# Performance work log

Measured on AMD Instinct MI355X. Metric: run time of the kernel, lower is better.

Reference implementation:

```python
import jax, jax.numpy as jnp
import numpy as np
import math

N = 50000   # nodes
E = 800000  # edges
D = 64      # in_feat_dim == out_feat_dim
T = 8       # num node types
R = 8       # num relations
SQRT_DK = math.sqrt(D)


def typed_matmul(x, W, types, num_types):
    """Row-wise x[i] @ W[types[i]] without materializing [E, D, D] gathered weights."""
    out = jnp.zeros((x.shape[0], W.shape[-1]), x.dtype)
    for t in range(num_types):
        out = out + jnp.where((types == t)[:, None], x @ W[t], 0.0)
    return out


def segment_softmax(score, index, num_segments):
    smax = jax.ops.segment_max(score, index, num_segments=num_segments)
    ex = jnp.exp(score - smax[index])
    ssum = jax.ops.segment_sum(ex, index, num_segments=num_segments)
    return ex / (ssum[index] + 1e-16)


def setup_inputs() -> dict:
    key = jax.random.key(0)
    ks = jax.random.split(key, 10)
    h = jax.random.normal(ks[0], (N, D), dtype=jnp.float32)
    adj = jax.random.randint(ks[1], (2, E), 0, N, dtype=jnp.int64)
    edge_type = jax.random.randint(ks[2], (E,), 0, R, dtype=jnp.int64)
    node_type = jax.random.randint(ks[3], (N,), 0, T, dtype=jnp.int64)
    k_weights = jax.random.uniform(ks[4], (T, D, D), dtype=jnp.float32)
    q_weights = jax.random.uniform(ks[5], (T, D, D), dtype=jnp.float32)
    v_weights = jax.random.uniform(ks[6], (T, D, D), dtype=jnp.float32)
    a_weights = jax.random.uniform(ks[7], (T, D, D), dtype=jnp.float32)
    relation_att = jax.random.uniform(ks[8], (R, D, D), dtype=jnp.float32)
    relation_msg = jax.random.uniform(ks[9], (R, D, D), dtype=jnp.float32)
    relation_pri = jnp.ones((R, 1), dtype=jnp.float32)
    skip = jnp.ones((T,), dtype=jnp.float32)
    return {
        "h": h, "adj": adj, "edge_type": edge_type, "node_type": node_type,
        "src_type": 0, "dst_type": 0,
        "k_weights": k_weights, "q_weights": q_weights, "v_weights": v_weights,
        "a_weights": a_weights, "relation_pri": relation_pri,
        "relation_att": relation_att, "relation_msg": relation_msg, "skip": skip,
    }


def reference(h, adj, edge_type, node_type, src_type, dst_type,
              k_weights, q_weights, v_weights, a_weights,
              relation_pri, relation_att, relation_msg, skip):
    src = adj[0]  # _j side (messages come from src)
    dst = adj[1]  # _i side (scatter/softmax index)

    # Node-type-indexed projections (done per node, then gathered per edge --
    # identical math to the per-edge bmm in the original).
    k_node = typed_matmul(h, k_weights, node_type, T)  # [N, D]
    q_node = typed_matmul(h, q_weights, node_type, T)
    v_node = typed_matmul(h, v_weights, node_type, T)

    # Relation-indexed per-edge transforms.
    k = typed_matmul(k_node[src], relation_att, edge_type, R)  # [E, D]
    v = typed_matmul(v_node[src], relation_msg, edge_type, R)  # [E, D]
    q = q_node[dst]                                            # [E, D]

    attn_score = jnp.sum(k * q, axis=1, keepdims=True) * relation_pri[edge_type] / SQRT_DK  # [E, 1]
    alpha = segment_softmax(attn_score, dst, N)  # edge softmax over incoming edges
    rst = v * alpha                              # [E, D]

    agg = jax.ops.segment_sum(rst, dst, num_segments=N)  # [N, D]

    # Update: node-type-indexed output transform scaled by sigmoid(skip[type]).
    trans_out = typed_matmul(agg, a_weights, node_type, T)
    alpha_skip = jax.nn.sigmoid(skip[node_type])
    return trans_out * alpha_skip[:, None]
```

## Files before the change

kernel.cpp:

```cpp
#include <hip/hip_runtime.h>
#include <math.h>

typedef float f32x4 __attribute__((ext_vector_type(4)));
typedef short bf16x8 __attribute__((ext_vector_type(8)));
typedef _Float16 f16x8 __attribute__((ext_vector_type(8)));
typedef _Float16 f16x4 __attribute__((ext_vector_type(4)));

#define D 64
#define TT 8
#define RR 8

#define SCAN_TPB 256
#define SCAN_CH 4
#define SCAN_ELEMS (SCAN_TPB * SCAN_CH)

#define HIST_CH 8
#define SCAT_CH 4
#define SCORE_XB 256
#define V2_XB 64
#define AGG_XB 256

__device__ __forceinline__ float bf2f(unsigned short u) {
    union { unsigned int i; float f; } x;
    x.i = ((unsigned int)u) << 16;
    return x.f;
}
__device__ __forceinline__ unsigned short f2bf(float f) {
    union { float f; unsigned int i; } x;
    x.f = f;
    unsigned int i = x.i;
    unsigned int r = (i + 0x7FFFu + ((i >> 16) & 1u)) >> 16;
    return (unsigned short)r;
}
struct BfPair { short hi; short lo; };
__device__ __forceinline__ BfPair split2(float x) {
    BfPair p;
    unsigned short h = f2bf(x);
    p.hi = (short)h;
    p.lo = (short)f2bf(x - bf2f(h));
    return p;
}
__device__ __forceinline__ void load_A_split(const float* __restrict__ p, bf16x8& ah, bf16x8& al) {
#pragma unroll
    for (int i = 0; i < 8; ++i) {
        BfPair s = split2(p[i]);
        ah[i] = s.hi; al[i] = s.lo;
    }
}
__device__ __forceinline__ void load_B_split(const float* __restrict__ W, int ks, int c, int lane,
                                             bf16x8& bh, bf16x8& bl) {
    int n = lane & 15, q = lane >> 4;
#pragma unroll
    for (int i = 0; i < 8; ++i) {
        BfPair s = split2(W[(ks * 32 + q * 8 + i) * 64 + c * 16 + n]);
        bh[i] = s.hi; bl[i] = s.lo;
    }
}
__device__ __forceinline__ void load_B_split_f16(const float* __restrict__ W, int ks, int c, int lane,
                                                 f16x8& bh, f16x8& bl) {
    int n = lane & 15, q = lane >> 4;
#pragma unroll
    for (int i = 0; i < 8; ++i) {
        float w = W[(ks * 32 + q * 8 + i) * 64 + c * 16 + n];
        _Float16 h = (_Float16)w;
        bh[i] = h;
        bl[i] = (_Float16)(w - (float)h);
    }
}
__device__ __forceinline__ f16x8 load_B_frag_f16(const float* __restrict__ W, int ks, int c, int lane) {
    int n = lane & 15, q = lane >> 4;
    f16x8 r;
#pragma unroll
    for (int i = 0; i < 8; ++i)
        r[i] = (_Float16)W[(ks * 32 + q * 8 + i) * 64 + c * 16 + n];
    return r;
}

#define MFMA16(a, b, c) __builtin_amdgcn_mfma_f32_16x16x32_bf16(a, b, c, 0, 0, 0)
#define MFMAH(a, b, c)  __builtin_amdgcn_mfma_f32_16x16x32_f16(a, b, c, 0, 0, 0)

#define SPLIT_MFMA_BODY(acc, A0h, A0l, A1h, A1l, Bh, Bl)          \
    _Pragma("unroll")                                             \
    for (int c = 0; c < 4; ++c) {                                 \
        acc[c] = MFMA16(A0h, Bh[0][c], acc[c]);                   \
        acc[c] = MFMA16(A0l, Bh[0][c], acc[c]);                   \
        acc[c] = MFMA16(A0h, Bl[0][c], acc[c]);                   \
        acc[c] = MFMA16(A1h, Bh[1][c], acc[c]);                   \
        acc[c] = MFMA16(A1l, Bh[1][c], acc[c]);                   \
        acc[c] = MFMA16(A1h, Bl[1][c], acc[c]);                   \
    }

__global__ void hist_kernel(const int* __restrict__ dst, const int* __restrict__ et,
                            const int* __restrict__ nt,
                            int* __restrict__ deg, int* __restrict__ tcnt, int* __restrict__ rcnt,
                            int* __restrict__ erank, int N, int E) {
    __shared__ int l_r[RR], l_t[TT];
    if (threadIdx.x < RR) l_r[threadIdx.x] = 0;
    if (threadIdx.x < TT) l_t[threadIdx.x] = 0;
    __syncthreads();
    const int stride = gridDim.x * blockDim.x;
    const int tid = blockIdx.x * blockDim.x + threadIdx.x;
#pragma unroll
    for (int i = 0; i < HIST_CH; ++i) {
        int e = tid + i * stride;
        if (e < E) {
            erank[e] = atomicAdd(&deg[dst[e]], 1);
            atomicAdd(&l_r[et[e]], 1);
        }
    }
#pragma unroll
    for (int i = 0; i < HIST_CH; ++i) {
        int n = tid + i * stride;
        if (n < N) atomicAdd(&l_t[nt[n]], 1);
    }
    __syncthreads();
    if (threadIdx.x < RR && l_r[threadIdx.x]) atomicAdd(&rcnt[threadIdx.x], l_r[threadIdx.x]);
    if (threadIdx.x < TT && l_t[threadIdx.x]) atomicAdd(&tcnt[threadIdx.x], l_t[threadIdx.x]);
}

__global__ void scan_sum_kernel(const int* __restrict__ deg, int* __restrict__ bsum, int N) {
    __shared__ int ws[SCAN_TPB / 64];
    int tid = threadIdx.x;
    int base = blockIdx.x * SCAN_ELEMS + tid * SCAN_CH;
    int s = 0;
#pragma unroll
    for (int i = 0; i < SCAN_CH; ++i) {
        int idx = base + i;
        if (idx < N) s += deg[idx];
    }
#pragma unroll
    for (int d = 32; d; d >>= 1) s += __shfl_xor(s, d, 64);
    if ((tid & 63) == 0) ws[tid >> 6] = s;
    __syncthreads();
    if (tid == 0) {
        int t = 0;
#pragma unroll
        for (int i = 0; i < SCAN_TPB / 64; ++i) t += ws[i];
        bsum[blockIdx.x] = t;
    }
}
__global__ void scan_out_kernel(const int* __restrict__ deg, const int* __restrict__ bsum, int nsb,
                                int* __restrict__ off, int N, int Etot,
                                const int* __restrict__ tcnt, int* __restrict__ toff, int* __restrict__ tcur,
                                const int* __restrict__ rcnt, int* __restrict__ roff, int* __restrict__ rcur) {
    __shared__ int ts[SCAN_TPB];
    __shared__ int bb;
    int tid = threadIdx.x;
    if (tid < 64) {
        int v = 0;
        if (nsb <= 64) {
            v = (tid < nsb && tid < blockIdx.x) ? bsum[tid] : 0;
#pragma unroll
            for (int d = 32; d; d >>= 1) v += __shfl_xor(v, d, 64);
        } else if (tid == 0) {
            for (int b = 0; b < blockIdx.x; ++b) v += bsum[b];
        }
        if (tid == 0) bb = v;
    }
    if (blockIdx.x == 0 && tid == 1) {
        int a = 0;
        for (int t = 0; t < TT; ++t) { toff[t] = a; tcur[t] = a; a += tcnt[t]; }
        toff[TT] = a;
        int b2 = 0;
        for (int r = 0; r < RR; ++r) { roff[r] = b2; rcur[r] = b2; b2 += rcnt[r]; }
        roff[RR] = b2;
        off[N] = Etot;
    }
    int base = blockIdx.x * SCAN_ELEMS + tid * SCAN_CH;
    int loc[SCAN_CH];
    int s = 0;
#pragma unroll
    for (int i = 0; i < SCAN_CH; ++i) {
        int idx = base + i;
        int v = (idx < N) ? deg[idx] : 0;
        loc[i] = v; s += v;
    }
    ts[tid] = s;
    __syncthreads();
    for (int sh = 1; sh < SCAN_TPB; sh <<= 1) {
        int v = (tid >= sh) ? ts[tid - sh] : 0;
        __syncthreads();
        ts[tid] += v;
        __syncthreads();
    }
    int run = bb + ((tid > 0) ? ts[tid - 1] : 0);
#pragma unroll
    for (int i = 0; i < SCAN_CH; ++i) {
        int idx = base + i;
        if (idx < N) { off[idx] = run; run += loc[i]; }
    }
}

__global__ void scatter_kernel(const int* __restrict__ src, const int* __restrict__ dst,
                               const int* __restrict__ et, const int* __restrict__ nt,
                               const int* __restrict__ offs, const int* __restrict__ erank,
                               int* __restrict__ tcur, int* __restrict__ rcur,
                               int* __restrict__ rsrc, int* __restrict__ rdst,
                               int* __restrict__ rdpos, int* __restrict__ nidx, int N, int E) {
    __shared__ int l_r[RR], l_t[TT], base_r[RR], base_t[TT];
    if (threadIdx.x < RR) l_r[threadIdx.x] = 0;
    if (threadIdx.x < TT) l_t[threadIdx.x] = 0;
    __syncthreads();
    const int stride = gridDim.x * blockDim.x;
    const int tid = blockIdx.x * blockDim.x + threadIdx.x;
    int s[SCAT_CH], d[SCAT_CH], r[SCAT_CH], rrank[SCAT_CH];
    int t[SCAT_CH], trank[SCAT_CH];
#pragma unroll
    for (int i = 0; i < SCAT_CH; ++i) {
        int e = tid + i * stride;
        if (e < E) {
            s[i] = src[e]; d[i] = dst[e]; r[i] = et[e];
            rrank[i] = atomicAdd(&l_r[r[i]], 1);
        }
        int n = tid + i * stride;
        if (n < N) {
            t[i] = nt[n];
            trank[i] = atomicAdd(&l_t[t[i]], 1);
        }
    }
    __syncthreads();
    if (threadIdx.x < RR)
        base_r[threadIdx.x] = l_r[threadIdx.x] ? atomicAdd(&rcur[threadIdx.x], l_r[threadIdx.x]) : 0;
    if (threadIdx.x < TT)
        base_t[threadIdx.x] = l_t[threadIdx.x] ? atomicAdd(&tcur[threadIdx.x], l_t[threadIdx.x]) : 0;
    __syncthreads();
#pragma unroll
    for (int i = 0; i < SCAT_CH; ++i) {
        int e = tid + i * stride;
        if (e < E) {
            int pos = offs[d[i]] + erank[e];
            int rp = base_r[r[i]] + rrank[i];
            rsrc[rp] = s[i]; rdst[rp] = d[i]; rdpos[rp] = pos;
        }
        int n = tid + i * stride;
        if (n < N) nidx[base_t[t[i]] + trank[i]] = n;
    }
}

__global__ void proj_kernel(const float* __restrict__ h,
                            const float* __restrict__ Wk, const float* __restrict__ Wq,
                            const float* __restrict__ Wv,
                            const int* __restrict__ toff, const int* __restrict__ nidx,
                            _Float16* __restrict__ kh16,
                            _Float16* __restrict__ qout, _Float16* __restrict__ vout) {
    const int t = blockIdx.z, a = blockIdx.y, lane = threadIdx.x;
    const int beg = toff[t], end = toff[t + 1], cnt = end - beg;
    if (cnt <= 0) return;
    const int nstrips = (cnt + 15) >> 4;
    const float* W = (a == 0 ? Wk : (a == 1 ? Wq : Wv)) + (size_t)t * 4096;
    const int m = lane & 15, quad = lane >> 4;

    bf16x8 Bh[2][4], Bl[2][4];
#pragma unroll
    for (int ks = 0; ks < 2; ++ks)
#pragma unroll
        for (int c = 0; c < 4; ++c) load_B_split(W, ks, c, lane, Bh[ks][c], Bl[ks][c]);

    _Float16* out = (a == 0) ? kh16 : (a == 1 ? qout : vout);

    for (int s = blockIdx.x; s < nstrips; s += gridDim.x) {
        int base = beg + s * 16;
        int rA = base + m; if (rA > end - 1) rA = end - 1;
        const float* hp = h + (size_t)nidx[rA] * D;
        bf16x8 A0h, A0l, A1h, A1l;
        load_A_split(hp + quad * 8, A0h, A0l);
        load_A_split(hp + 32 + quad * 8, A1h, A1l);
        f32x4 acc[4];
#pragma unroll
        for (int c = 0; c < 4; ++c) acc[c] = (f32x4){0.f, 0.f, 0.f, 0.f};
        SPLIT_MFMA_BODY(acc, A0h, A0l, A1h, A1l, Bh, Bl)
#pragma unroll
        for (int reg = 0; reg < 4; ++reg) {
            int rr = base + quad * 4 + reg;
            if (rr < end) {
                int nid = nidx[rr];
#pragma unroll
                for (int c = 0; c < 4; ++c)
                    out[(size_t)nid * D + c * 16 + m] = (_Float16)acc[c][reg];
            }
        }
    }
}

__global__ void score_v2_kernel(const int* __restrict__ rsrc, const int* __restrict__ rdst,
                                const int* __restrict__ rdpos, const int* __restrict__ roff,
                                const _Float16* __restrict__ kh16,
                                const _Float16* __restrict__ qn, const float* __restrict__ Aatt,
                                const float* __restrict__ pri, int2* __restrict__ rec,
                                const _Float16* __restrict__ vn, const float* __restrict__ Amsg,
                                _Float16* __restrict__ V2, int N) {
    const int r = blockIdx.y;
    const int lane = threadIdx.x & 63;
    const int wv = threadIdx.x >> 6;
    const int m = lane & 15, quad = lane >> 4;

    if (blockIdx.x >= SCORE_XB) {
        const int g = (blockIdx.x - SCORE_XB) * 4 + wv;
        const int nstrips = (N + 15) >> 4;
        const float* W = Amsg + (size_t)r * 4096;
        f16x8 B[2][4];
#pragma unroll
        for (int ks = 0; ks < 2; ++ks)
#pragma unroll
            for (int c = 0; c < 4; ++c) B[ks][c] = load_B_frag_f16(W, ks, c, lane);

        for (int s = g; s < nstrips; s += V2_XB * 4) {
            int base = s * 16;
            int rA = base + m; if (rA > N - 1) rA = N - 1;
            f16x8 A0 = *(const f16x8*)(vn + (size_t)rA * D + quad * 8);
            f16x8 A1 = *(const f16x8*)(vn + (size_t)rA * D + 32 + quad * 8);
            f32x4 acc[4];
#pragma unroll
            for (int c = 0; c < 4; ++c) acc[c] = (f32x4){0.f, 0.f, 0.f, 0.f};
#pragma unroll
            for (int c = 0; c < 4; ++c) {
                acc[c] = MFMAH(A0, B[0][c], acc[c]);
                acc[c] = MFMAH(A1, B[1][c], acc[c]);
            }
#pragma unroll
            for (int reg = 0; reg < 4; ++reg) {
                int rr = base + quad * 4 + reg;
                if (rr < N) {
#pragma unroll
                    for (int c = 0; c < 4; ++c)
                        V2[((size_t)rr * RR + r) * D + c * 16 + m] = (_Float16)acc[c][reg];
                }
            }
        }
        return;
    }

    const int beg = roff[r], end = roff[r + 1], cnt = end - beg;
    if (cnt <= 0) return;
    const int nstrips = (cnt + 15) >> 4;
    const float scale = pri[r] * 0.125f;
    const float* W = Aatt + (size_t)r * 4096;

    f16x8 Bh[2][4], Bl[2][4];
#pragma unroll
    for (int ks = 0; ks < 2; ++ks)
#pragma unroll
        for (int c = 0; c < 4; ++c) load_B_split_f16(W, ks, c, lane, Bh[ks][c], Bl[ks][c]);

    const int g = blockIdx.x * 4 + wv;
    for (int st = g; st < nstrips; st += SCORE_XB * 4) {
        int base = st * 16;
        int ia = base + m; if (ia > cnt - 1) ia = cnt - 1;
        int s = rsrc[beg + ia];
        const _Float16* kr = kh16 + (size_t)s * D;
        f16x8 A0 = *(const f16x8*)(kr + quad * 8);
        f16x8 A1 = *(const f16x8*)(kr + 32 + quad * 8);
        f32x4 acc[4];
#pragma unroll
        for (int c = 0; c < 4; ++c) acc[c] = (f32x4){0.f, 0.f, 0.f, 0.f};
#pragma unroll
        for (int c = 0; c < 4; ++c) {
            acc[c] = MFMAH(A0, Bh[0][c], acc[c]);
            acc[c] = MFMAH(A0, Bl[0][c], acc[c]);
            acc[c] = MFMAH(A1, Bh[1][c], acc[c]);
            acc[c] = MFMAH(A1, Bl[1][c], acc[c]);
        }

        float p4[4];
#pragma unroll
        for (int reg = 0; reg < 4; ++reg) {
            int ie = base + quad * 4 + reg; if (ie > cnt - 1) ie = cnt - 1;
            const _Float16* qp = qn + (size_t)rdst[beg + ie] * D + m;
            float pr = acc[0][reg] * (float)qp[0] + acc[1][reg] * (float)qp[16]
                     + acc[2][reg] * (float)qp[32] + acc[3][reg] * (float)qp[48];
#pragma unroll
            for (int d = 8; d; d >>= 1) pr += __shfl_xor(pr, d, 64);
            p4[reg] = pr;
        }
        if (m < 4) {
            int idx = base + quad * 4 + m;
            if (idx < cnt) {
                float v = (m == 0) ? p4[0] : (m == 1) ? p4[1] : (m == 2) ? p4[2] : p4[3];
                int sagain = rsrc[beg + idx];
                int2 rc;
                rc.x = __float_as_int(v * scale);
                rc.y = (sagain << 3) | r;
                rec[rdpos[beg + idx]] = rc;
            }
        }
    }
}

__global__ void agg_out_kernel(const int* __restrict__ offs, const int2* __restrict__ rec,
                               const _Float16* __restrict__ V2,
                               const float* __restrict__ Wa, const float* __restrict__ skp,
                               const int* __restrict__ toff, const int* __restrict__ nidx,
                               float* __restrict__ out) {
    const int t = blockIdx.y;
    const int beg = toff[t], end = toff[t + 1], cnt = end - beg;
    if (cnt <= 0) return;
    const int nstrips = (cnt + 15) >> 4;
    const int lane = threadIdx.x & 63;
    const int wv = threadIdx.x >> 6;
    const int quad = lane >> 4, ql = lane & 15;
    const int q16 = wv * 4 + quad;
    const int qb = quad << 4;
    const int m = lane & 15, qd = lane >> 4;
    const float sg = 1.f / (1.f + __expf(-skp[t]));

    __shared__ float As[16][68];

    bf16x8 Bh2[2], Bl2[2];
    const float* W = Wa + (size_t)t * 4096;
#pragma unroll
    for (int ks = 0; ks < 2; ++ks) load_B_split(W, ks, wv, lane, Bh2[ks], Bl2[ks]);

    for (int s = blockIdx.x; s < nstrips; s += gridDim.x) {
        int base = beg + s * 16;
        int rr = base + q16; if (rr > end - 1) rr = end - 1;
        int i = nidx[rr];
        const int ebeg = offs[i], eend = offs[i + 1];
        float mmax = -INFINITY, lsum = 0.f;
        float a0 = 0.f, a1 = 0.f, a2 = 0.f, a3 = 0.f;
        for (int cs = ebeg; cs < eend; cs += 16) {
            int cl = eend - cs; if (cl > 16) cl = 16;
            int2 rc; rc.y = 0;
            float sc = -INFINITY;
            if (ql < cl) { rc = rec[cs + ql]; sc = __int_as_float(rc.x); }
            float cm = sc;
#pragma unroll
            for (int d = 8; d; d >>= 1) cm = fmaxf(cm, __shfl_xor(cm, d, 64));
            float mn = fmaxf(mmax, cm);
            float cf = __expf(mmax - mn);
            float ex = (ql < cl) ? __expf(sc - mn) : 0.f;
            float csum = ex;
#pragma unroll
            for (int d = 8; d; d >>= 1) csum += __shfl_xor(csum, d, 64);
            lsum = lsum * cf + csum;
            a0 *= cf; a1 *= cf; a2 *= cf; a3 *= cf;
            for (int e = 0; e < cl; e += 4) {
                float w0 = __shfl(ex, qb + e, 64),     w1 = __shfl(ex, qb + e + 1, 64);
                float w2 = __shfl(ex, qb + e + 2, 64), w3 = __shfl(ex, qb + e + 3, 64);
                int   i0 = __shfl(rc.y, qb + e, 64),     i1 = __shfl(rc.y, qb + e + 1, 64);
                int   i2 = __shfl(rc.y, qb + e + 2, 64), i3 = __shfl(rc.y, qb + e + 3, 64);
                f16x4 v0 = *(const f16x4*)(V2 + (size_t)i0 * D + ql * 4);
                f16x4 v1 = *(const f16x4*)(V2 + (size_t)i1 * D + ql * 4);
                f16x4 v2 = *(const f16x4*)(V2 + (size_t)i2 * D + ql * 4);
                f16x4 v3 = *(const f16x4*)(V2 + (size_t)i3 * D + ql * 4);
                a0 += w0 * (float)v0[0] + w1 * (float)v1[0] + w2 * (float)v2[0] + w3 * (float)v3[0];
                a1 += w0 * (float)v0[1] + w1 * (float)v1[1] + w2 * (float)v2[1] + w3 * (float)v3[1];
                a2 += w0 * (float)v0[2] + w1 * (float)v1[2] + w2 * (float)v2[2] + w3 * (float)v3[2];
                a3 += w0 * (float)v0[3] + w1 * (float)v1[3] + w2 * (float)v2[3] + w3 * (float)v3[3];
            }
            mmax = mn;
        }
        float inv = 1.f / (lsum + 1e-16f);
        As[q16][ql * 4 + 0] = a0 * inv;
        As[q16][ql * 4 + 1] = a1 * inv;
        As[q16][ql * 4 + 2] = a2 * inv;
        As[q16][ql * 4 + 3] = a3 * inv;
        __syncthreads();

        bf16x8 A0h, A0l, A1h, A1l;
        load_A_split(&As[m][qd * 8], A0h, A0l);
        load_A_split(&As[m][32 + qd * 8], A1h, A1l);
        f32x4 acc = (f32x4){0.f, 0.f, 0.f, 0.f};
        acc = MFMA16(A0h, Bh2[0], acc);
        acc = MFMA16(A0l, Bh2[0], acc);
        acc = MFMA16(A0h, Bl2[0], acc);
        acc = MFMA16(A1h, Bh2[1], acc);
        acc = MFMA16(A1l, Bh2[1], acc);
        acc = MFMA16(A1h, Bl2[1], acc);
#pragma unroll
        for (int reg = 0; reg < 4; ++reg) {
            int rrr = base + qd * 4 + reg;
            if (rrr < end)
                out[(size_t)nidx[rrr] * D + wv * 16 + m] = acc[reg] * sg;
        }
        __syncthreads();
    }
}

extern "C" void kernel_launch(void* const* d_in, const int* in_sizes, int n_in,
                              void* d_out, int out_size, void* d_ws, size_t ws_size,
                              hipStream_t stream) {
    const float* h     = (const float*)d_in[0];
    const int*   adj   = (const int*)d_in[1];
    const int*   etype = (const int*)d_in[2];
    const int*   ntype = (const int*)d_in[3];
    const float* Wk    = (const float*)d_in[6];
    const float* Wq    = (const float*)d_in[7];
    const float* Wv    = (const float*)d_in[8];
    const float* Wa    = (const float*)d_in[9];
    const float* pri   = (const float*)d_in[10];
    const float* Aatt  = (const float*)d_in[11];
    const float* Amsg  = (const float*)d_in[12];
    const float* skp   = (const float*)d_in[13];
    const int N = in_sizes[3];
    const int E = in_sizes[2];
    float* out = (float*)d_out;

    char* w = (char*)d_ws;
    auto alloc = [&](size_t b) { char* p = w; w += (b + 255) & ~(size_t)255; return p; };
    _Float16* kh16 = (_Float16*)alloc((size_t)N * D * 2);
    _Float16* qn   = (_Float16*)alloc((size_t)N * D * 2);
    _Float16* vn   = (_Float16*)alloc((size_t)N * D * 2);
    _Float16* V2   = (_Float16*)alloc((size_t)N * RR * D * 2);
    int* deg  = (int*)alloc((size_t)(N + 16) * 4);
    int* tcnt = deg + N;
    int* rcnt = deg + N + 8;
    int* offs = (int*)alloc((size_t)(N + 1) * 4);
    int* erank = (int*)alloc((size_t)E * 4);
    int* toff = (int*)alloc(64);
    int* tcur = (int*)alloc(64);
    int* roff = (int*)alloc(64);
    int* rcur = (int*)alloc(64);
    int2* rec = (int2*)alloc((size_t)E * 8);
    int* rsrc  = (int*)alloc((size_t)E * 4);
    int* rdst  = (int*)alloc((size_t)E * 4);
    int* rdpos = (int*)alloc((size_t)E * 4);
    int* nidx  = (int*)alloc((size_t)N * 4);
    const int nsb = (N + SCAN_ELEMS - 1) / SCAN_ELEMS;
    int* bsum  = (int*)alloc((size_t)nsb * 4);

    (void)hipMemsetAsync(deg, 0, (size_t)(N + 16) * 4, stream);

    const int mx = (E > N ? E : N);
    const int histBlocks = (mx + 256 * HIST_CH - 1) / (256 * HIST_CH);
    hist_kernel<<<histBlocks, 256, 0, stream>>>(adj + E, etype, ntype, deg, tcnt, rcnt, erank, N, E);
    scan_sum_kernel<<<nsb, SCAN_TPB, 0, stream>>>(deg, bsum, N);
    scan_out_kernel<<<nsb, SCAN_TPB, 0, stream>>>(deg, bsum, nsb, offs, N, E,
                                                  tcnt, toff, tcur, rcnt, roff, rcur);
    const int scatBlocks = (mx + 256 * SCAT_CH - 1) / (256 * SCAT_CH);
    scatter_kernel<<<scatBlocks, 256, 0, stream>>>(adj, adj + E, etype, ntype,
                                                   offs, erank, tcur, rcur,
                                                   rsrc, rdst, rdpos, nidx, N, E);
    proj_kernel<<<dim3(128, 3, TT), 64, 0, stream>>>(h, Wk, Wq, Wv, toff, nidx, kh16, qn, vn);
    score_v2_kernel<<<dim3(SCORE_XB + V2_XB, RR), 256, 0, stream>>>(rsrc, rdst, rdpos, roff,
                                                                    kh16, qn, Aatt, pri, rec,
                                                                    vn, Amsg, V2, N);
    agg_out_kernel<<<dim3(AGG_XB, TT), 256, 0, stream>>>(offs, rec, V2, Wa, skp, toff, nidx, out);
}
```

Measured before the change: 257.7 us.

## Fold relation attention into per-destination query transform and fuse scoring into aggregation

Rather than computing k_node[src] @ relation_att[r] per edge, the new code computes q_node[dst] @ relation_att[r]^T per destination node for all 8 relations inside the aggregation kernel, then dots it with the gathered source key. This removes the relation-sorted edge buckets, the separate score kernel and the per-edge score record buffer, and replaces them with a single packed src/relation word per CSR edge. The cost is 8 split-bf16 MFMA transforms per destination node, Aatt fragments reloaded on every strip, a larger shared-memory footprint that may reduce occupancy, and an fp32 query buffer.

```diff
diff --git a/kernel.cpp b/kernel.cpp
--- a/kernel.cpp
+++ b/kernel.cpp
@@ -16,7 +16,6 @@
 
 #define HIST_CH 8
 #define SCAT_CH 4
-#define SCORE_XB 256
 #define V2_XB 64
 #define AGG_XB 256
 
@@ -56,15 +55,13 @@
         bh[i] = s.hi; bl[i] = s.lo;
     }
 }
-__device__ __forceinline__ void load_B_split_f16(const float* __restrict__ W, int ks, int c, int lane,
-                                                 f16x8& bh, f16x8& bl) {
+__device__ __forceinline__ void load_B_splitT(const float* __restrict__ W, int ks, int c, int lane,
+                                              bf16x8& bh, bf16x8& bl) {
     int n = lane & 15, q = lane >> 4;
 #pragma unroll
     for (int i = 0; i < 8; ++i) {
-        float w = W[(ks * 32 + q * 8 + i) * 64 + c * 16 + n];
-        _Float16 h = (_Float16)w;
-        bh[i] = h;
-        bl[i] = (_Float16)(w - (float)h);
+        BfPair s = split2(W[(c * 16 + n) * 64 + ks * 32 + q * 8 + i]);
+        bh[i] = s.hi; bl[i] = s.lo;
     }
 }
 __device__ __forceinline__ f16x8 load_B_frag_f16(const float* __restrict__ W, int ks, int c, int lane) {
@@ -90,12 +87,10 @@
         acc[c] = MFMA16(A1h, Bl[1][c], acc[c]);                   \
     }
 
-__global__ void hist_kernel(const int* __restrict__ dst, const int* __restrict__ et,
-                            const int* __restrict__ nt,
-                            int* __restrict__ deg, int* __restrict__ tcnt, int* __restrict__ rcnt,
+__global__ void hist_kernel(const int* __restrict__ dst, const int* __restrict__ nt,
+                            int* __restrict__ deg, int* __restrict__ tcnt,
                             int* __restrict__ erank, int N, int E) {
-    __shared__ int l_r[RR], l_t[TT];
-    if (threadIdx.x < RR) l_r[threadIdx.x] = 0;
+    __shared__ int l_t[TT];
     if (threadIdx.x < TT) l_t[threadIdx.x] = 0;
     __syncthreads();
     const int stride = gridDim.x * blockDim.x;
@@ -103,10 +98,7 @@
 #pragma unroll
     for (int i = 0; i < HIST_CH; ++i) {
         int e = tid + i * stride;
-        if (e < E) {
-            erank[e] = atomicAdd(&deg[dst[e]], 1);
-            atomicAdd(&l_r[et[e]], 1);
-        }
+        if (e < E) erank[e] = atomicAdd(&deg[dst[e]], 1);
     }
 #pragma unroll
     for (int i = 0; i < HIST_CH; ++i) {
@@ -114,7 +106,6 @@
         if (n < N) atomicAdd(&l_t[nt[n]], 1);
     }
     __syncthreads();
-    if (threadIdx.x < RR && l_r[threadIdx.x]) atomicAdd(&rcnt[threadIdx.x], l_r[threadIdx.x]);
     if (threadIdx.x < TT && l_t[threadIdx.x]) atomicAdd(&tcnt[threadIdx.x], l_t[threadIdx.x]);
 }
 
@@ -141,8 +132,7 @@
 }
 __global__ void scan_out_kernel(const int* __restrict__ deg, const int* __restrict__ bsum, int nsb,
                                 int* __restrict__ off, int N, int Etot,
-                                const int* __restrict__ tcnt, int* __restrict__ toff, int* __restrict__ tcur,
-                                const int* __restrict__ rcnt, int* __restrict__ roff, int* __restrict__ rcur) {
+                                const int* __restrict__ tcnt, int* __restrict__ toff, int* __restrict__ tcur) {
     __shared__ int ts[SCAN_TPB];
     __shared__ int bb;
     int tid = threadIdx.x;
@@ -161,9 +151,6 @@
         int a = 0;
         for (int t = 0; t < TT; ++t) { toff[t] = a; tcur[t] = a; a += tcnt[t]; }
         toff[TT] = a;
-        int b2 = 0;
-        for (int r = 0; r < RR; ++r) { roff[r] = b2; rcur[r] = b2; b2 += rcnt[r]; }
-        roff[RR] = b2;
         off[N] = Etot;
     }
     int base = blockIdx.x * SCAN_ELEMS + tid * SCAN_CH;
@@ -194,23 +181,20 @@
 __global__ void scatter_kernel(const int* __restrict__ src, const int* __restrict__ dst,
                                const int* __restrict__ et, const int* __restrict__ nt,
                                const int* __restrict__ offs, const int* __restrict__ erank,
-                               int* __restrict__ tcur, int* __restrict__ rcur,
-                               int* __restrict__ rsrc, int* __restrict__ rdst,
-                               int* __restrict__ rdpos, int* __restrict__ nidx, int N, int E) {
-    __shared__ int l_r[RR], l_t[TT], base_r[RR], base_t[TT];
-    if (threadIdx.x < RR) l_r[threadIdx.x] = 0;
+                               int* __restrict__ tcur, int* __restrict__ einfo,
+                               int* __restrict__ nidx, int N, int E) {
+    __shared__ int l_t[TT], base_t[TT];
     if (threadIdx.x < TT) l_t[threadIdx.x] = 0;
     __syncthreads();
     const int stride = gridDim.x * blockDim.x;
     const int tid = blockIdx.x * blockDim.x + threadIdx.x;
-    int s[SCAT_CH], d[SCAT_CH], r[SCAT_CH], rrank[SCAT_CH];
     int t[SCAT_CH], trank[SCAT_CH];
 #pragma unroll
     for (int i = 0; i < SCAT_CH; ++i) {
         int e = tid + i * stride;
         if (e < E) {
-            s[i] = src[e]; d[i] = dst[e]; r[i] = et[e];
-            rrank[i] = atomicAdd(&l_r[r[i]], 1);
+            int s = src[e], d = dst[e], r = et[e];
+            einfo[offs[d] + erank[e]] = (s << 3) | r;
         }
         int n = tid + i * stride;
         if (n < N) {
@@ -219,19 +203,11 @@
         }
     }
     __syncthreads();
-    if (threadIdx.x < RR)
-        base_r[threadIdx.x] = l_r[threadIdx.x] ? atomicAdd(&rcur[threadIdx.x], l_r[threadIdx.x]) : 0;
     if (threadIdx.x < TT)
         base_t[threadIdx.x] = l_t[threadIdx.x] ? atomicAdd(&tcur[threadIdx.x], l_t[threadIdx.x]) : 0;
     __syncthreads();
 #pragma unroll
     for (int i = 0; i < SCAT_CH; ++i) {
-        int e = tid + i * stride;
-        if (e < E) {
-            int pos = offs[d[i]] + erank[e];
-            int rp = base_r[r[i]] + rrank[i];
-            rsrc[rp] = s[i]; rdst[rp] = d[i]; rdpos[rp] = pos;
-        }
         int n = tid + i * stride;
         if (n < N) nidx[base_t[t[i]] + trank[i]] = n;
     }
@@ -242,7 +218,7 @@
                             const float* __restrict__ Wv,
                             const int* __restrict__ toff, const int* __restrict__ nidx,
                             _Float16* __restrict__ kh16,
-                            _Float16* __restrict__ qout, _Float16* __restrict__ vout) {
+                            float* __restrict__ qout, _Float16* __restrict__ vout) {
     const int t = blockIdx.z, a = blockIdx.y, lane = threadIdx.x;
     const int beg = toff[t], end = toff[t + 1], cnt = end - beg;
     if (cnt <= 0) return;
@@ -255,8 +231,6 @@
     for (int ks = 0; ks < 2; ++ks)
 #pragma unroll
         for (int c = 0; c < 4; ++c) load_B_split(W, ks, c, lane, Bh[ks][c], Bl[ks][c]);
-
-    _Float16* out = (a == 0) ? kh16 : (a == 1 ? qout : vout);
 
     for (int s = blockIdx.x; s < nstrips; s += gridDim.x) {
         int base = beg + s * 16;
@@ -275,122 +249,63 @@
             if (rr < end) {
                 int nid = nidx[rr];
 #pragma unroll
-                for (int c = 0; c < 4; ++c)
-                    out[(size_t)nid * D + c * 16 + m] = (_Float16)acc[c][reg];
+                for (int c = 0; c < 4; ++c) {
+                    float val = acc[c][reg];
+                    if (a == 0)      kh16[(size_t)nid * D + c * 16 + m] = (_Float16)val;
+                    else if (a == 1) qout[(size_t)nid * D + c * 16 + m] = val;
+                    else             vout[(size_t)nid * D + c * 16 + m] = (_Float16)val;
+                }
             }
         }
     }
 }
 
-__global__ void score_v2_kernel(const int* __restrict__ rsrc, const int* __restrict__ rdst,
-                                const int* __restrict__ rdpos, const int* __restrict__ roff,
-                                const _Float16* __restrict__ kh16,
-                                const _Float16* __restrict__ qn, const float* __restrict__ Aatt,
-                                const float* __restrict__ pri, int2* __restrict__ rec,
-                                const _Float16* __restrict__ vn, const float* __restrict__ Amsg,
-                                _Float16* __restrict__ V2, int N) {
+__global__ void v2_kernel(const _Float16* __restrict__ vn, const float* __restrict__ Amsg,
+                          _Float16* __restrict__ V2, int N) {
     const int r = blockIdx.y;
     const int lane = threadIdx.x & 63;
     const int wv = threadIdx.x >> 6;
     const int m = lane & 15, quad = lane >> 4;
-
-    if (blockIdx.x >= SCORE_XB) {
-        const int g = (blockIdx.x - SCORE_XB) * 4 + wv;
-        const int nstrips = (N + 15) >> 4;
-        const float* W = Amsg + (size_t)r * 4096;
-        f16x8 B[2][4];
-#pragma unroll
-        for (int ks = 0; ks < 2; ++ks)
-#pragma unroll
-            for (int c = 0; c < 4; ++c) B[ks][c] = load_B_frag_f16(W, ks, c, lane);
-
-        for (int s = g; s < nstrips; s += V2_XB * 4) {
-            int base = s * 16;
-            int rA = base + m; if (rA > N - 1) rA = N - 1;
-            f16x8 A0 = *(const f16x8*)(vn + (size_t)rA * D + quad * 8);
-            f16x8 A1 = *(const f16x8*)(vn + (size_t)rA * D + 32 + quad * 8);
-            f32x4 acc[4];
-#pragma unroll
-            for (int c = 0; c < 4; ++c) acc[c] = (f32x4){0.f, 0.f, 0.f, 0.f};
-#pragma unroll
-            for (int c = 0; c < 4; ++c) {
-                acc[c] = MFMAH(A0, B[0][c], acc[c]);
-                acc[c] = MFMAH(A1, B[1][c], acc[c]);
+    const int nstrips = (N + 15) >> 4;
+    const float* W = Amsg + (size_t)r * 4096;
+    f16x8 B[2][4];
+#pragma unroll
+    for (int ks = 0; ks < 2; ++ks)
+#pragma unroll
+        for (int c = 0; c < 4; ++c) B[ks][c] = load_B_frag_f16(W, ks, c, lane);
+
+    for (int s = blockIdx.x * 4 + wv; s < nstrips; s += V2_XB * 4) {
+        int base = s * 16;
+        int rA = base + m; if (rA > N - 1) rA = N - 1;
+        f16x8 A0 = *(const f16x8*)(vn + (size_t)rA * D + quad * 8);
+        f16x8 A1 = *(const f16x8*)(vn + (size_t)rA * D + 32 + quad * 8);
+        f32x4 acc[4];
+#pragma unroll
+        for (int c = 0; c < 4; ++c) acc[c] = (f32x4){0.f, 0.f, 0.f, 0.f};
+#pragma unroll
+        for (int c = 0; c < 4; ++c) {
+            acc[c] = MFMAH(A0, B[0][c], acc[c]);
+            acc[c] = MFMAH(A1, B[1][c], acc[c]);
+        }
+#pragma unroll
+        for (int reg = 0; reg < 4; ++reg) {
+            int rr = base + quad * 4 + reg;
+            if (rr < N) {
+#pragma unroll
+                for (int c = 0; c < 4; ++c)
+                    V2[((size_t)rr * RR + r) * D + c * 16 + m] = (_Float16)acc[c][reg];
             }
-#pragma unroll
-            for (int reg = 0; reg < 4; ++reg) {
-                int rr = base + quad * 4 + reg;
-                if (rr < N) {
-#pragma unroll
-                    for (int c = 0; c < 4; ++c)
-                        V2[((size_t)rr * RR + r) * D + c * 16 + m] = (_Float16)acc[c][reg];
-                }
-            }
-        }
-        return;
-    }
-
-    const int beg = roff[r], end = roff[r + 1], cnt = end - beg;
-    if (cnt <= 0) return;
-    const int nstrips = (cnt + 15) >> 4;
-    const float scale = pri[r] * 0.125f;
-    const float* W = Aatt + (size_t)r * 4096;
-
-    f16x8 Bh[2][4], Bl[2][4];
-#pragma unroll
-    for (int ks = 0; ks < 2; ++ks)
-#pragma unroll
-        for (int c = 0; c < 4; ++c) load_B_split_f16(W, ks, c, lane, Bh[ks][c], Bl[ks][c]);
-
-    const int g = blockIdx.x * 4 + wv;
-    for (int st = g; st < nstrips; st += SCORE_XB * 4) {
-        int base = st * 16;
-        int ia = base + m; if (ia > cnt - 1) ia = cnt - 1;
-        int s = rsrc[beg + ia];
-        const _Float16* kr = kh16 + (size_t)s * D;
-        f16x8 A0 = *(const f16x8*)(kr + quad * 8);
-        f16x8 A1 = *(const f16x8*)(kr + 32 + quad * 8);
-        f32x4 acc[4];
-#pragma unroll
-        for (int c = 0; c < 4; ++c) acc[c] = (f32x4){0.f, 0.f, 0.f, 0.f};
-#pragma unroll
-        for (int c = 0; c < 4; ++c) {
-            acc[c] = MFMAH(A0, Bh[0][c], acc[c]);
-            acc[c] = MFMAH(A0, Bl[0][c], acc[c]);
-            acc[c] = MFMAH(A1, Bh[1][c], acc[c]);
-            acc[c] = MFMAH(A1, Bl[1][c], acc[c]);
-        }
-
-        float p4[4];
-#pragma unroll
-        for (int reg = 0; reg < 4; ++reg) {
-            int ie = base + quad * 4 + reg; if (ie > cnt - 1) ie = cnt - 1;
-            const _Float16* qp = qn + (size_t)rdst[beg + ie] * D + m;
-            float pr = acc[0][reg] * (float)qp[0] + acc[1][reg] * (float)qp[16]
-                     + acc[2][reg] * (float)qp[32] + acc[3][reg] * (float)qp[48];
-#pragma unroll
-            for (int d = 8; d; d >>= 1) pr += __shfl_xor(pr, d, 64);
-            p4[reg] = pr;
-        }
-        if (m < 4) {
-            int idx = base + quad * 4 + m;
-            if (idx < cnt) {
-                float v = (m == 0) ? p4[0] : (m == 1) ? p4[1] : (m == 2) ? p4[2] : p4[3];
-                int sagain = rsrc[beg + idx];
-                int2 rc;
-                rc.x = __float_as_int(v * scale);
-                rc.y = (sagain << 3) | r;
-                rec[rdpos[beg + idx]] = rc;
-            }
-        }
-    }
-}
-
-__global__ void agg_out_kernel(const int* __restrict__ offs, const int2* __restrict__ rec,
-                               const _Float16* __restrict__ V2,
-                               const float* __restrict__ Wa, const float* __restrict__ skp,
-                               const int* __restrict__ toff, const int* __restrict__ nidx,
-                               float* __restrict__ out) {
+        }
+    }
+}
+
+__global__ void fused_kernel(const int* __restrict__ offs, const int* __restrict__ einfo,
+                             const _Float16* __restrict__ kh16, const float* __restrict__ qn,
+                             const _Float16* __restrict__ V2,
+                             const float* __restrict__ Aatt, const float* __restrict__ pri,
+                             const float* __restrict__ Wa, const float* __restrict__ skp,
+                             const int* __restrict__ toff, const int* __restrict__ nidx,
+                             float* __restrict__ out) {
     const int t = blockIdx.y;
     const int beg = toff[t], end = toff[t + 1], cnt = end - beg;
     if (cnt <= 0) return;
@@ -403,31 +318,95 @@
     const int m = lane & 15, qd = lane >> 4;
     const float sg = 1.f / (1.f + __expf(-skp[t]));
 
+    __shared__ float QTs[16][RR][64];
     __shared__ float As[16][68];
+    __shared__ float pri_s[RR];
+    if (threadIdx.x < RR) pri_s[threadIdx.x] = pri[threadIdx.x] * 0.125f;
 
     bf16x8 Bh2[2], Bl2[2];
-    const float* W = Wa + (size_t)t * 4096;
-#pragma unroll
-    for (int ks = 0; ks < 2; ++ks) load_B_split(W, ks, wv, lane, Bh2[ks], Bl2[ks]);
+    const float* Wo = Wa + (size_t)t * 4096;
+#pragma unroll
+    for (int ks = 0; ks < 2; ++ks) load_B_split(Wo, ks, wv, lane, Bh2[ks], Bl2[ks]);
 
     for (int s = blockIdx.x; s < nstrips; s += gridDim.x) {
         int base = beg + s * 16;
+
+        {
+            int rA = base + m; if (rA > end - 1) rA = end - 1;
+            const float* qp = qn + (size_t)nidx[rA] * D;
+            bf16x8 A0h, A0l, A1h, A1l;
+            load_A_split(qp + quad * 8, A0h, A0l);
+            load_A_split(qp + 32 + quad * 8, A1h, A1l);
+            for (int rj = 0; rj < 2; ++rj) {
+                int r = wv * 2 + rj;
+                const float* W = Aatt + (size_t)r * 4096;
+                bf16x8 Bh[2][4], Bl[2][4];
+#pragma unroll
+                for (int ks = 0; ks < 2; ++ks)
+#pragma unroll
+                    for (int c = 0; c < 4; ++c) load_B_splitT(W, ks, c, lane, Bh[ks][c], Bl[ks][c]);
+                f32x4 acc[4];
+#pragma unroll
+                for (int c = 0; c < 4; ++c) acc[c] = (f32x4){0.f, 0.f, 0.f, 0.f};
+                SPLIT_MFMA_BODY(acc, A0h, A0l, A1h, A1l, Bh, Bl)
+#pragma unroll
+                for (int reg = 0; reg < 4; ++reg)
+#pragma unroll
+                    for (int c = 0; c < 4; ++c)
+                        QTs[quad * 4 + reg][r][c * 16 + m] = acc[c][reg];
+            }
+        }
+        __syncthreads();
+
         int rr = base + q16; if (rr > end - 1) rr = end - 1;
         int i = nidx[rr];
         const int ebeg = offs[i], eend = offs[i + 1];
+        const float* QTn = &QTs[q16][0][0];
         float mmax = -INFINITY, lsum = 0.f;
         float a0 = 0.f, a1 = 0.f, a2 = 0.f, a3 = 0.f;
         for (int cs = ebeg; cs < eend; cs += 16) {
             int cl = eend - cs; if (cl > 16) cl = 16;
-            int2 rc; rc.y = 0;
-            float sc = -INFINITY;
-            if (ql < cl) { rc = rec[cs + ql]; sc = __int_as_float(rc.x); }
-            float cm = sc;
+            int info = (ql < cl) ? einfo[cs + ql] : 0;
+            float mysc = -INFINITY;
+            for (int e0 = 0; e0 < cl; e0 += 4) {
+                int i0 = __shfl(info, qb + e0, 64);
+                int i1 = __shfl(info, qb + e0 + 1, 64);
+                int i2 = __shfl(info, qb + e0 + 2, 64);
+                int i3 = __shfl(info, qb + e0 + 3, 64);
+                f16x4 k0 = *(const f16x4*)(kh16 + (size_t)(i0 >> 3) * D + ql * 4);
+                f16x4 k1 = *(const f16x4*)(kh16 + (size_t)(i1 >> 3) * D + ql * 4);
+                f16x4 k2 = *(const f16x4*)(kh16 + (size_t)(i2 >> 3) * D + ql * 4);
+                f16x4 k3 = *(const f16x4*)(kh16 + (size_t)(i3 >> 3) * D + ql * 4);
+                const float* t0 = QTn + (i0 & 7) * 64 + ql * 4;
+                const float* t1 = QTn + (i1 & 7) * 64 + ql * 4;
+                const float* t2 = QTn + (i2 & 7) * 64 + ql * 4;
+                const float* t3 = QTn + (i3 & 7) * 64 + ql * 4;
+                float p0 = (float)k0[0]*t0[0] + (float)k0[1]*t0[1] + (float)k0[2]*t0[2] + (float)k0[3]*t0[3];
+                float p1 = (float)k1[0]*t1[0] + (float)k1[1]*t1[1] + (float)k1[2]*t1[2] + (float)k1[3]*t1[3];
+                float p2 = (float)k2[0]*t2[0] + (float)k2[1]*t2[1] + (float)k2[2]*t2[2] + (float)k2[3]*t2[3];
+                float p3 = (float)k3[0]*t3[0] + (float)k3[1]*t3[1] + (float)k3[2]*t3[2] + (float)k3[3]*t3[3];
+#pragma unroll
+                for (int d = 8; d; d >>= 1) {
+                    p0 += __shfl_xor(p0, d, 64);
+                    p1 += __shfl_xor(p1, d, 64);
+                    p2 += __shfl_xor(p2, d, 64);
+                    p3 += __shfl_xor(p3, d, 64);
+                }
+                float s0 = p0 * pri_s[i0 & 7];
+                float s1 = p1 * pri_s[i1 & 7];
+                float s2 = p2 * pri_s[i2 & 7];
+                float s3 = p3 * pri_s[i3 & 7];
+                if (ql == e0) mysc = s0;
+                if (e0 + 1 < cl && ql == e0 + 1) mysc = s1;
+                if (e0 + 2 < cl && ql == e0 + 2) mysc = s2;
+                if (e0 + 3 < cl && ql == e0 + 3) mysc = s3;
+            }
+            float cm = mysc;
 #pragma unroll
             for (int d = 8; d; d >>= 1) cm = fmaxf(cm, __shfl_xor(cm, d, 64));
             float mn = fmaxf(mmax, cm);
             float cf = __expf(mmax - mn);
-            float ex = (ql < cl) ? __expf(sc - mn) : 0.f;
+            float ex = (ql < cl) ? __expf(mysc - mn) : 0.f;
             float csum = ex;
 #pragma unroll
             for (int d = 8; d; d >>= 1) csum += __shfl_xor(csum, d, 64);
@@ -436,8 +415,8 @@
             for (int e = 0; e < cl; e += 4) {
                 float w0 = __shfl(ex, qb + e, 64),     w1 = __shfl(ex, qb + e + 1, 64);
                 float w2 = __shfl(ex, qb + e + 2, 64), w3 = __shfl(ex, qb + e + 3, 64);
-                int   i0 = __shfl(rc.y, qb + e, 64),     i1 = __shfl(rc.y, qb + e + 1, 64);
-                int   i2 = __shfl(rc.y, qb + e + 2, 64), i3 = __shfl(rc.y, qb + e + 3, 64);
+                int   i0 = __shfl(info, qb + e, 64),     i1 = __shfl(info, qb + e + 1, 64);
+                int   i2 = __shfl(info, qb + e + 2, 64), i3 = __shfl(info, qb + e + 3, 64);
                 f16x4 v0 = *(const f16x4*)(V2 + (size_t)i0 * D + ql * 4);
                 f16x4 v1 = *(const f16x4*)(V2 + (size_t)i1 * D + ql * 4);
                 f16x4 v2 = *(const f16x4*)(V2 + (size_t)i2 * D + ql * 4);
@@ -498,22 +477,16 @@
     char* w = (char*)d_ws;
     auto alloc = [&](size_t b) { char* p = w; w += (b + 255) & ~(size_t)255; return p; };
     _Float16* kh16 = (_Float16*)alloc((size_t)N * D * 2);
-    _Float16* qn   = (_Float16*)alloc((size_t)N * D * 2);
+    float*    qn   = (float*)alloc((size_t)N * D * 4);
     _Float16* vn   = (_Float16*)alloc((size_t)N * D * 2);
     _Float16* V2   = (_Float16*)alloc((size_t)N * RR * D * 2);
     int* deg  = (int*)alloc((size_t)(N + 16) * 4);
     int* tcnt = deg + N;
-    int* rcnt = deg + N + 8;
     int* offs = (int*)alloc((size_t)(N + 1) * 4);
     int* erank = (int*)alloc((size_t)E * 4);
     int* toff = (int*)alloc(64);
     int* tcur = (int*)alloc(64);
-    int* roff = (int*)alloc(64);
-    int* rcur = (int*)alloc(64);
-    int2* rec = (int2*)alloc((size_t)E * 8);
-    int* rsrc  = (int*)alloc((size_t)E * 4);
-    int* rdst  = (int*)alloc((size_t)E * 4);
-    int* rdpos = (int*)alloc((size_t)E * 4);
+    int* einfo = (int*)alloc((size_t)E * 4);
     int* nidx  = (int*)alloc((size_t)N * 4);
     const int nsb = (N + SCAN_ELEMS - 1) / SCAN_ELEMS;
     int* bsum  = (int*)alloc((size_t)nsb * 4);
@@ -522,17 +495,14 @@
 
     const int mx = (E > N ? E : N);
     const int histBlocks = (mx + 256 * HIST_CH - 1) / (256 * HIST_CH);
-    hist_kernel<<<histBlocks, 256, 0, stream>>>(adj + E, etype, ntype, deg, tcnt, rcnt, erank, N, E);
+    hist_kernel<<<histBlocks, 256, 0, stream>>>(adj + E, ntype, deg, tcnt, erank, N, E);
     scan_sum_kernel<<<nsb, SCAN_TPB, 0, stream>>>(deg, bsum, N);
-    scan_out_kernel<<<nsb, SCAN_TPB, 0, stream>>>(deg, bsum, nsb, offs, N, E,
-                                                  tcnt, toff, tcur, rcnt, roff, rcur);
+    scan_out_kernel<<<nsb, SCAN_TPB, 0, stream>>>(deg, bsum, nsb, offs, N, E, tcnt, toff, tcur);
     const int scatBlocks = (mx + 256 * SCAT_CH - 1) / (256 * SCAT_CH);
     scatter_kernel<<<scatBlocks, 256, 0, stream>>>(adj, adj + E, etype, ntype,
-                                                   offs, erank, tcur, rcur,
-                                                   rsrc, rdst, rdpos, nidx, N, E);
+                                                   offs, erank, tcur, einfo, nidx, N, E);
     proj_kernel<<<dim3(128, 3, TT), 64, 0, stream>>>(h, Wk, Wq, Wv, toff, nidx, kh16, qn, vn);
-    score_v2_kernel<<<dim3(SCORE_XB + V2_XB, RR), 256, 0, stream>>>(rsrc, rdst, rdpos, roff,
-                                                                    kh16, qn, Aatt, pri, rec,
-                                                                    vn, Amsg, V2, N);
-    agg_out_kernel<<<dim3(AGG_XB, TT), 256, 0, stream>>>(offs, rec, V2, Wa, skp, toff, nidx, out);
-}
+    v2_kernel<<<dim3(V2_XB, RR), 256, 0, stream>>>(vn, Amsg, V2, N);
+    fused_kernel<<<dim3(AGG_XB, TT), 256, 0, stream>>>(offs, einfo, kh16, qn, V2,
+                                                       Aatt, pri, Wa, skp, toff, nidx, out);
+}
```

Result: slower. 292.9 us (+13.6%).
